# Performance work log

Measured on AMD Instinct MI355X. Metric: run time of the kernel, lower is better.

The kernel has to match this reference:

```python
import jax, jax.numpy as jnp
import numpy as np

B, T, D, H, C = 1024, 128, 13, 512, 9
EPS = 1e-5


def _layer_norm(x, g, b):
    m = x.mean(-1, keepdims=True)
    v = ((x - m) ** 2).mean(-1, keepdims=True)
    return (x - m) / jnp.sqrt(v + EPS) * g + b


def _batch_norm(x, g, b):
    # x: (B, T, H); BatchNorm1d over channel H -> stats over (B, T), biased var
    m = x.mean((0, 1))
    v = ((x - m) ** 2).mean((0, 1))
    return (x - m) / jnp.sqrt(v + EPS) * g + b


def _star_layer(x, WxK, bxK, Wxz, bxz, WhK, bhK, bn_g, bn_b):
    # Precompute input projections for all timesteps (batched GEMMs)
    xK = jnp.einsum('btd,hd->bth', x, WxK) + bxK          # (B,T,H)
    z = jnp.tanh(jnp.einsum('btd,hd->bth', x, Wxz) + bxz)  # (B,T,H)
    h0 = jnp.zeros((x.shape[0], WhK.shape[0]), x.dtype)

    def step(h, inp):
        gK, zt = inp
        K = jax.nn.sigmoid(gK + h @ WhK.T + bhK)
        hn = jnp.tanh(K * h + (1.0 - K) * zt)
        return hn, hn

    _, outs = jax.lax.scan(step, h0, (xK.swapaxes(0, 1), z.swapaxes(0, 1)))
    outs = outs.swapaxes(0, 1)  # (B,T,H)
    return _batch_norm(outs, bn_g, bn_b)


def setup_inputs() -> dict:
    key = jax.random.key(0)
    ks = jax.random.split(key, 10)

    def w(k, o, i):
        return jax.random.normal(k, (o, i), jnp.float32) / np.sqrt(i)

    return {
        'x': jax.random.normal(ks[0], (B, T, D), jnp.float32),
        'inln_g': jnp.ones((D,), jnp.float32),
        'inln_b': jnp.zeros((D,), jnp.float32),
        # layer 1 (input_dim -> H)
        'WxK1': w(ks[1], H, D), 'bxK1': jnp.ones((H,), jnp.float32),
        'Wxz1': w(ks[2], H, D), 'bxz1': jnp.zeros((H,), jnp.float32),
        'WhK1': w(ks[3], H, H), 'bhK1': jnp.zeros((H,), jnp.float32),
        'bn1_g': jnp.ones((H,), jnp.float32), 'bn1_b': jnp.zeros((H,), jnp.float32),
        # layer 2 == layer 3 (shared module instance in the original Sequential)
        'WxK2': w(ks[4], H, H), 'bxK2': jnp.ones((H,), jnp.float32),
        'Wxz2': w(ks[5], H, H), 'bxz2': jnp.zeros((H,), jnp.float32),
        'WhK2': w(ks[6], H, H), 'bhK2': jnp.zeros((H,), jnp.float32),
        'bn2_g': jnp.ones((H,), jnp.float32), 'bn2_b': jnp.zeros((H,), jnp.float32),
        'cln_g': jnp.ones((H,), jnp.float32), 'cln_b': jnp.zeros((H,), jnp.float32),
        'Wc': w(ks[7], C, H), 'bc': jnp.zeros((C,), jnp.float32),
    }


def reference(x, inln_g, inln_b,
              WxK1, bxK1, Wxz1, bxz1, WhK1, bhK1, bn1_g, bn1_b,
              WxK2, bxK2, Wxz2, bxz2, WhK2, bhK2, bn2_g, bn2_b,
              cln_g, cln_b, Wc, bc):
    x = _layer_norm(x, inln_g, inln_b)
    o = _star_layer(x, WxK1, bxK1, Wxz1, bxz1, WhK1, bhK1, bn1_g, bn1_b)
    # layers 2 and 3 share the same weights and batchnorm (duplicated module)
    o = _star_layer(o, WxK2, bxK2, Wxz2, bxz2, WhK2, bhK2, bn2_g, bn2_b)
    o = _star_layer(o, WxK2, bxK2, Wxz2, bxz2, WhK2, bhK2, bn2_g, bn2_b)
    h = _layer_norm(o[:, -1, :], cln_g, cln_b)
    logits = h @ Wc.T + bc
    return jax.nn.log_softmax(logits, axis=-1)
```

## Files before the change

kernel.cpp:

```cpp
#include <hip/hip_runtime.h>
#include <hip/hip_bf16.h>
#include <math.h>

#define B_ 1024
#define T_ 128
#define D_ 13
#define H_ 512
#define C_ 9
#define TC_ 32
#define NC_ (T_/TC_)
#define NT_ (B_*T_)
#define EPS 1e-5f
#define WPAD 520

using frag_ab = __attribute__((ext_vector_type(8))) short;
using frag_cd = __attribute__((ext_vector_type(4))) float;
typedef unsigned short ushort8 __attribute__((ext_vector_type(8)));

static __device__ __forceinline__ float bf2f(unsigned short u){
  union { unsigned int i; float f; } v; v.i = ((unsigned int)u)<<16; return v.f;
}
static __device__ __forceinline__ unsigned short f2bf(float f){
  union { float f; unsigned int i; } v; v.f = f;
  unsigned int r = v.i + 0x7FFF + ((v.i >> 16) & 1);
  return (unsigned short)(r >> 16);
}
static __device__ __forceinline__ float sigmoidf_(float x){ return 1.0f/(1.0f+__expf(-x)); }
static __device__ __forceinline__ float tanhf_(float x){
  return 1.0f - 2.0f/(__expf(2.0f*x)+1.0f);
}

__global__ void k_zero(unsigned int* __restrict__ p, int n){
  int i=blockIdx.x*256+threadIdx.x; if(i<n) p[i]=0u;
}

__global__ void k_swz(const float* __restrict__ Wf, unsigned short* __restrict__ Wz){
  int dst = blockIdx.x*256 + threadIdx.x;
  int w = dst >> 15;
  int i = (dst >> 9) & 63;
  int L = (dst >> 3) & 63;
  int e = dst & 7;
  int kc = i >> 2, c = i & 3;
  int row = w*64 + c*16 + (L & 15);
  int col = kc*32 + ((L >> 4) << 3) + e;
  Wz[dst] = f2bf(Wf[row*H_ + col]);
}

__global__ __launch_bounds__(256) void k_proj1(
    const float* __restrict__ x, const float* __restrict__ g, const float* __restrict__ bvec,
    const float* __restrict__ WxK, const float* __restrict__ bxK,
    const float* __restrict__ Wxz, const float* __restrict__ bxz,
    unsigned short* __restrict__ xKo, unsigned short* __restrict__ zo, int t0)
{
  __shared__ float wK[H_*D_];
  __shared__ float wz[H_*D_];
  __shared__ float xn[TC_][D_];
  int tid = threadIdx.x;
  int b = blockIdx.x;
  const float* xin = x + ((size_t)b*T_ + t0)*D_;
  for(int i=tid;i<H_*D_;i+=256){ wK[i]=WxK[i]; wz[i]=Wxz[i]; }
  for(int i=tid;i<TC_*D_;i+=256){ ((float*)xn)[i] = xin[i]; }
  __syncthreads();
  if(tid<TC_){
    float m=0.f; for(int d=0;d<D_;++d) m+=xn[tid][d]; m*=(1.0f/D_);
    float v=0.f; for(int d=0;d<D_;++d){float t=xn[tid][d]-m; v+=t*t;} v*=(1.0f/D_);
    float inv = rsqrtf(v+EPS);
    for(int d=0;d<D_;++d) xn[tid][d] = (xn[tid][d]-m)*inv*g[d]+bvec[d];
  }
  __syncthreads();
  size_t ob = (size_t)b*TC_*H_;
  for(int hh=0; hh<2; ++hh){
    int h = tid + hh*256;
    float bK = bxK[h], bz = bxz[h];
    for(int r=0;r<TC_;++r){
      float aK=bK, az=bz;
      #pragma unroll
      for(int d=0;d<D_;++d){ float xv = xn[r][d]; aK += xv*wK[h*D_+d]; az += xv*wz[h*D_+d]; }
      xKo[ob + (size_t)r*H_ + h] = f2bf(aK);
      zo [ob + (size_t)r*H_ + h] = f2bf(tanhf_(az));
    }
  }
}

__global__ __launch_bounds__(1024,1) void k_recur8(
    const unsigned short* __restrict__ xK, const unsigned short* __restrict__ z,
    const unsigned short* __restrict__ Wz,
    const float* __restrict__ bhK,
    unsigned short* __restrict__ o,
    float* __restrict__ hbuf,
    float* __restrict__ stats, int t0)
{
  __shared__ __align__(16) unsigned short Wl[8*15*512];
  __shared__ __align__(16) unsigned short hbd[2][16*WPAD];
  int tid=threadIdx.x, lane=tid&63, w=tid>>6;
  int ow=w>>1, oh=w&1;
  int q=lane>>4, cl=lane&15;
  int b0 = blockIdx.x*16;
  const unsigned short* wb = Wz + ((size_t)ow<<15);
  const unsigned short* wl = Wl + ow*7680;
  for(int j=tid;j<7680;j+=1024){
    int wv = j/960, off8 = j%960;
    *(ushort8*)&Wl[wv*7680 + off8*8] = *(const ushort8*)&Wz[((size_t)wv<<15) + off8*8];
  }
  float hp[8];
  float bh[2]; int col[2];
  float ss[2]={0.f,0.f}, qq[2]={0.f,0.f};
  #pragma unroll
  for(int c=0;c<2;++c){ col[c]=ow*64 + (oh*2+c)*16 + cl; bh[c]=bhK[col[c]]; }
  if(t0==0){
    for(int i=tid;i<16*WPAD;i+=1024) hbd[0][i]=0;
    #pragma unroll
    for(int i=0;i<8;++i) hp[i]=0.f;
  } else {
    for(int i=tid;i<16*H_;i+=1024){ int r=i>>9,c=i&511; hbd[0][r*WPAD+c]=f2bf(hbuf[(size_t)(b0+r)*H_+c]); }
    #pragma unroll
    for(int c=0;c<2;++c)
      #pragma unroll
      for(int rg=0;rg<4;++rg) hp[c*4+rg]=hbuf[(size_t)(b0+q*4+rg)*H_+col[c]];
  }
  __syncthreads();
  for(int dt=0;dt<TC_;++dt){
    int cb = dt&1, nb = cb^1;
    float ga[8], za[8];
    #pragma unroll
    for(int c=0;c<2;++c)
      #pragma unroll
      for(int rg=0;rg<4;++rg){
        size_t gi = ((size_t)(b0+q*4+rg)*TC_ + dt)*H_ + col[c];
        ga[c*4+rg]=bf2f(xK[gi]); za[c*4+rg]=bf2f(z[gi]);
      }
    frag_cd acc[2] = {};
    #pragma unroll
    for(int kc=0;kc<16;++kc){
      frag_ab af = *(const frag_ab*)&hbd[cb][cl*WPAD + kc*32 + q*8];
      #pragma unroll
      for(int c=0;c<2;++c){
        int f = kc*4 + oh*2 + c;
        frag_ab bf = (f<15) ? *(const frag_ab*)&wl[f*512 + lane*8]
                            : *(const frag_ab*)&wb[f*512 + lane*8];
        acc[c] = __builtin_amdgcn_mfma_f32_16x16x32_bf16(af, bf, acc[c], 0,0,0);
      }
    }
    unsigned short hnb[8];
    #pragma unroll
    for(int c=0;c<2;++c){
      #pragma unroll
      for(int rg=0;rg<4;++rg){
        int idx = c*4+rg;
        float gv = acc[c][rg] + bh[c] + ga[idx];
        float K  = sigmoidf_(gv);
        float hn = tanhf_(K*hp[idx] + (1.f-K)*za[idx]);
        hp[idx]=hn;
        hnb[idx]=f2bf(hn);
        hbd[nb][(q*4+rg)*WPAD + col[c]] = hnb[idx];
        float hf = bf2f(hnb[idx]);
        ss[c] += hf; qq[c] += hf*hf;
      }
    }
    __syncthreads();
    #pragma unroll
    for(int c=0;c<2;++c)
      #pragma unroll
      for(int rg=0;rg<4;++rg)
        o[((size_t)(b0+q*4+rg)*T_ + t0+dt)*H_ + col[c]] = hnb[c*4+rg];
  }
  #pragma unroll
  for(int c=0;c<2;++c)
    #pragma unroll
    for(int rg=0;rg<4;++rg) hbuf[(size_t)(b0+q*4+rg)*H_+col[c]] = hp[c*4+rg];
  #pragma unroll
  for(int c=0;c<2;++c){
    float s=ss[c], sq=qq[c];
    s  += __shfl_xor(s,16,64);  s  += __shfl_xor(s,32,64);
    sq += __shfl_xor(sq,16,64); sq += __shfl_xor(sq,32,64);
    if(q==0){ atomicAdd(&stats[col[c]], s); atomicAdd(&stats[H_+col[c]], sq); }
  }
}

__global__ void k_foldw(const float* __restrict__ WxK, const float* __restrict__ Wxz,
                        const float* __restrict__ stats, const float* __restrict__ bng,
                        unsigned short* __restrict__ Wp){
  int i = blockIdx.x*256+threadIdx.x;
  int n = i>>9, k = i&511;
  float mean = stats[k]*(1.f/NT_);
  float var  = stats[H_+k]*(1.f/NT_) - mean*mean;
  float s = bng[k]*rsqrtf(var+EPS);
  float wv = (n<H_) ? WxK[(size_t)n*H_+k] : Wxz[(size_t)(n-H_)*H_+k];
  Wp[i] = f2bf(wv*s);
}

__global__ __launch_bounds__(256) void k_foldb(const float* __restrict__ WxK, const float* __restrict__ Wxz,
                        const float* __restrict__ stats, const float* __restrict__ bng, const float* __restrict__ bnb,
                        const float* __restrict__ bxK, const float* __restrict__ bxz,
                        float* __restrict__ biasp){
  int w = threadIdx.x>>6, lane=threadIdx.x&63;
  int n = blockIdx.x*4 + w;
  const float* W = (n<H_) ? &WxK[(size_t)n*H_] : &Wxz[(size_t)(n-H_)*H_];
  float base = (n<H_) ? bxK[n] : bxz[n-H_];
  float acc=0.f;
  for(int k=lane;k<H_;k+=64){
    float mean = stats[k]*(1.f/NT_);
    float var  = stats[H_+k]*(1.f/NT_)-mean*mean;
    float s = bng[k]*rsqrtf(var+EPS);
    float t = bnb[k]-mean*s;
    acc += t*W[k];
  }
  for(int off=32;off;off>>=1) acc += __shfl_down(acc, off, 64);
  if(lane==0) biasp[n] = base + acc;
}

__global__ __launch_bounds__(256) void k_proj23(
    const unsigned short* __restrict__ A,
    const unsigned short* __restrict__ Wp,
    const float* __restrict__ biasp,
    unsigned short* __restrict__ xKo, unsigned short* __restrict__ zo, int t0)
{
  __shared__ __align__(16) unsigned short As[128*32];
  __shared__ __align__(16) unsigned short Bs[128*32];
  int tid=threadIdx.x, lane=tid&63, w=tid>>6;
  int q=lane>>4, cl=lane&15;
  int b0p = blockIdx.x*4;
  int n0 = blockIdx.y*128;
  int wm = (w>>1)*64, wn=(w&1)*64;
  frag_cd acc[4][4] = {};
  int sr = tid>>1, cb = (tid&1)*16;
  size_t arow = ((size_t)(b0p + (sr>>5))*T_ + t0 + (sr&31))*H_;
  size_t brow = (size_t)(n0+sr)*H_;
  for(int k0=0;k0<H_;k0+=32){
    *(frag_ab*)&As[sr*32+cb]   = *(const frag_ab*)&A [arow + k0+cb];
    *(frag_ab*)&As[sr*32+cb+8] = *(const frag_ab*)&A [arow + k0+cb+8];
    *(frag_ab*)&Bs[sr*32+cb]   = *(const frag_ab*)&Wp[brow + k0+cb];
    *(frag_ab*)&Bs[sr*32+cb+8] = *(const frag_ab*)&Wp[brow + k0+cb+8];
    __syncthreads();
    frag_ab af[4], bfr[4];
    #pragma unroll
    for(int mt=0;mt<4;++mt) af[mt]  = *(const frag_ab*)&As[(wm+mt*16+cl)*32 + q*8];
    #pragma unroll
    for(int nt=0;nt<4;++nt) bfr[nt] = *(const frag_ab*)&Bs[(wn+nt*16+cl)*32 + q*8];
    #pragma unroll
    for(int mt=0;mt<4;++mt)
      #pragma unroll
      for(int nt=0;nt<4;++nt)
        acc[mt][nt] = __builtin_amdgcn_mfma_f32_16x16x32_bf16(af[mt], bfr[nt], acc[mt][nt],0,0,0);
    __syncthreads();
  }
  #pragma unroll
  for(int nt=0;nt<4;++nt){
    int coln = n0+wn+nt*16+cl;
    float bp = biasp[coln];
    bool isz = coln>=H_;
    #pragma unroll
    for(int mt=0;mt<4;++mt){
      #pragma unroll
      for(int rg=0;rg<4;++rg){
        int rm = wm+mt*16+q*4+rg;
        size_t orow = (size_t)(b0p*TC_ + rm)*H_;
        float v = acc[mt][nt][rg] + bp;
        if(isz) zo [orow + coln-H_] = f2bf(tanhf_(v));
        else    xKo[orow + coln]    = f2bf(v);
      }
    }
  }
}

__global__ __launch_bounds__(512) void k_head(const unsigned short* __restrict__ o,
     const float* __restrict__ stats, const float* __restrict__ bng, const float* __restrict__ bnb,
     const float* __restrict__ clng, const float* __restrict__ clnb,
     const float* __restrict__ Wc, const float* __restrict__ bc, float* __restrict__ out)
{
  __shared__ float red[8];
  __shared__ float lred[8][9];
  int tid=threadIdx.x, lane=tid&63, w=tid>>6;
  int b = blockIdx.x;
  int c = tid;
  float v = bf2f(o[((size_t)b*T_ + (T_-1))*H_ + c]);
  float mean = stats[c]*(1.f/NT_), var = stats[H_+c]*(1.f/NT_)-mean*mean;
  float s = bng[c]*rsqrtf(var+EPS);
  float y = v*s + (bnb[c]-mean*s);
  float sm=y;
  for(int off=32;off;off>>=1) sm+=__shfl_down(sm,off,64);
  if(lane==0) red[w]=sm;
  __syncthreads();
  float mu=0.f; for(int i=0;i<8;++i) mu+=red[i]; mu*=(1.f/H_);
  float d = y-mu;
  float vq = d*d;
  for(int off=32;off;off>>=1) vq+=__shfl_down(vq,off,64);
  __syncthreads();
  if(lane==0) red[w]=vq;
  __syncthreads();
  float vv=0.f; for(int i=0;i<8;++i) vv+=red[i]; vv*=(1.f/H_);
  float yn = d*rsqrtf(vv+EPS)*clng[c]+clnb[c];
  for(int cls=0;cls<C_;++cls){
    float t = yn*Wc[(size_t)cls*H_+c];
    for(int off=32;off;off>>=1) t+=__shfl_down(t,off,64);
    if(lane==0) lred[w][cls]=t;
  }
  __syncthreads();
  if(tid==0){
    float lg[C_]; float mx=-1e30f;
    for(int cls=0;cls<C_;++cls){
      float t=bc[cls]; for(int i=0;i<8;++i) t+=lred[i][cls];
      lg[cls]=t; mx=fmaxf(mx,t);
    }
    float se=0.f; for(int cls=0;cls<C_;++cls) se+=__expf(lg[cls]-mx);
    float lse=mx+logf(se);
    for(int cls=0;cls<C_;++cls) out[(size_t)b*C_+cls]=lg[cls]-lse;
  }
}

extern "C" void kernel_launch(void* const* d_in, const int* in_sizes, int n_in,
                              void* d_out, int out_size, void* d_ws, size_t ws_size,
                              hipStream_t stream)
{
  (void)in_sizes; (void)n_in; (void)out_size; (void)ws_size;
  const float* x    =(const float*)d_in[0];
  const float* inlng=(const float*)d_in[1];
  const float* inlnb=(const float*)d_in[2];
  const float* WxK1 =(const float*)d_in[3];
  const float* bxK1 =(const float*)d_in[4];
  const float* Wxz1 =(const float*)d_in[5];
  const float* bxz1 =(const float*)d_in[6];
  const float* WhK1 =(const float*)d_in[7];
  const float* bhK1 =(const float*)d_in[8];
  const float* bn1g =(const float*)d_in[9];
  const float* bn1b =(const float*)d_in[10];
  const float* WxK2 =(const float*)d_in[11];
  const float* bxK2 =(const float*)d_in[12];
  const float* Wxz2 =(const float*)d_in[13];
  const float* bxz2 =(const float*)d_in[14];
  const float* WhK2 =(const float*)d_in[15];
  const float* bhK2 =(const float*)d_in[16];
  const float* bn2g =(const float*)d_in[17];
  const float* bn2b =(const float*)d_in[18];
  const float* clng =(const float*)d_in[19];
  const float* clnb =(const float*)d_in[20];
  const float* Wc   =(const float*)d_in[21];
  const float* bc   =(const float*)d_in[22];
  float* out=(float*)d_out;

  char* p=(char*)d_ws;
  unsigned short* o   =(unsigned short*)p; p+=(size_t)NT_*H_*2;
  unsigned short* xK  =(unsigned short*)p; p+=(size_t)B_*TC_*H_*2;
  unsigned short* z   =(unsigned short*)p; p+=(size_t)B_*TC_*H_*2;
  float* hbuf         =(float*)p;          p+=(size_t)B_*H_*4;
  unsigned short* Wz1 =(unsigned short*)p; p+=(size_t)H_*H_*2;
  unsigned short* Wz2 =(unsigned short*)p; p+=(size_t)H_*H_*2;
  unsigned short* Wp  =(unsigned short*)p; p+=(size_t)1024*H_*2;
  float* biasp        =(float*)p;          p+=1024*4;
  float* stats        =(float*)p;          p+=3*1024*4;

  k_zero<<<12,256,0,stream>>>((unsigned int*)stats, 3*1024);
  k_swz<<<H_*H_/256,256,0,stream>>>(WhK1, Wz1);
  k_swz<<<H_*H_/256,256,0,stream>>>(WhK2, Wz2);

  for(int c=0;c<NC_;++c){
    k_proj1<<<B_,256,0,stream>>>(x,inlng,inlnb,WxK1,bxK1,Wxz1,bxz1,xK,z,c*TC_);
    k_recur8<<<64,1024,0,stream>>>(xK,z,Wz1,bhK1,o,hbuf,stats,c*TC_);
  }

  k_foldw<<<1024*H_/256,256,0,stream>>>(WxK2,Wxz2,stats,bn1g,Wp);
  k_foldb<<<256,256,0,stream>>>(WxK2,Wxz2,stats,bn1g,bn1b,bxK2,bxz2,biasp);
  dim3 g23(B_/4, 8);
  for(int c=0;c<NC_;++c){
    k_proj23<<<g23,256,0,stream>>>(o,Wp,biasp,xK,z,c*TC_);
    k_recur8<<<64,1024,0,stream>>>(xK,z,Wz2,bhK2,o,hbuf,stats+1024,c*TC_);
  }

  k_foldw<<<1024*H_/256,256,0,stream>>>(WxK2,Wxz2,stats+1024,bn2g,Wp);
  k_foldb<<<256,256,0,stream>>>(WxK2,Wxz2,stats+1024,bn2g,bn2b,bxK2,bxz2,biasp);
  for(int c=0;c<NC_;++c){
    k_proj23<<<g23,256,0,stream>>>(o,Wp,biasp,xK,z,c*TC_);
    k_recur8<<<64,1024,0,stream>>>(xK,z,Wz2,bhK2,o,hbuf,stats+2048,c*TC_);
  }

  k_head<<<B_,512,0,stream>>>(o, stats+2048, bn2g,bn2b, clng,clnb, Wc,bc, out);
}
```

Before: 3.780 ms.

## Overlap next-chunk projection with recurrence in one fused kernel

Adds a fused kernel where the first 64 blocks run the recurrence for chunk k while up to 192 extra blocks compute the input projections for chunk k+1 into double-buffered xK/z buffers. The aim is to use idle CUs during the latency-bound recurrence and to cut the serialized proj/recur launches. It needs extra workspace and falls back to the old path when the workspace is too small. The projection blocks compete for bandwidth and may slow the recurrence blocks.

```diff
diff --git a/kernel.cpp b/kernel.cpp
--- a/kernel.cpp
+++ b/kernel.cpp
@@ -84,10 +84,8 @@
 
 __global__ __launch_bounds__(1024,1) void k_recur8(
     const unsigned short* __restrict__ xK, const unsigned short* __restrict__ z,
-    const unsigned short* __restrict__ Wz,
-    const float* __restrict__ bhK,
-    unsigned short* __restrict__ o,
-    float* __restrict__ hbuf,
+    const unsigned short* __restrict__ Wz, const float* __restrict__ bhK,
+    unsigned short* __restrict__ o, float* __restrict__ hbuf,
     float* __restrict__ stats, int t0)
 {
   __shared__ __align__(16) unsigned short Wl[8*15*512];
@@ -102,8 +100,7 @@
     int wv = j/960, off8 = j%960;
     *(ushort8*)&Wl[wv*7680 + off8*8] = *(const ushort8*)&Wz[((size_t)wv<<15) + off8*8];
   }
-  float hp[8];
-  float bh[2]; int col[2];
+  float hp[8]; float bh[2]; int col[2];
   float ss[2]={0.f,0.f}, qq[2]={0.f,0.f};
   #pragma unroll
   for(int c=0;c<2;++c){ col[c]=ow*64 + (oh*2+c)*16 + cl; bh[c]=bhK[col[c]]; }
@@ -174,6 +171,202 @@
     s  += __shfl_xor(s,16,64);  s  += __shfl_xor(s,32,64);
     sq += __shfl_xor(sq,16,64); sq += __shfl_xor(sq,32,64);
     if(q==0){ atomicAdd(&stats[col[c]], s); atomicAdd(&stats[H_+col[c]], sq); }
+  }
+}
+
+__global__ __launch_bounds__(1024,1) void k_fused(
+    const unsigned short* __restrict__ xKr, const unsigned short* __restrict__ zr,
+    const unsigned short* __restrict__ Wz, const float* __restrict__ bhK,
+    unsigned short* __restrict__ o, float* __restrict__ hbuf,
+    float* __restrict__ stats, int t0r,
+    int projKind,
+    const unsigned short* __restrict__ Wp, const float* __restrict__ biasp,
+    const float* __restrict__ x, const float* __restrict__ lng, const float* __restrict__ lnb,
+    const float* __restrict__ WxK, const float* __restrict__ bxK,
+    const float* __restrict__ Wxz, const float* __restrict__ bxz,
+    unsigned short* __restrict__ xKo, unsigned short* __restrict__ zo, int t0p)
+{
+  __shared__ __align__(16) unsigned char LDSB[156160];
+  int tid=threadIdx.x;
+  if(blockIdx.x < 64){
+    unsigned short* Wl  = (unsigned short*)LDSB;
+    unsigned short* hbd = (unsigned short*)(LDSB + 122880);
+    int lane=tid&63, w=tid>>6;
+    int ow=w>>1, oh=w&1;
+    int q=lane>>4, cl=lane&15;
+    int b0 = blockIdx.x*16;
+    const unsigned short* wb = Wz + ((size_t)ow<<15);
+    const unsigned short* wl = Wl + ow*7680;
+    for(int j=tid;j<7680;j+=1024){
+      int wv = j/960, off8 = j%960;
+      *(ushort8*)&Wl[wv*7680 + off8*8] = *(const ushort8*)&Wz[((size_t)wv<<15) + off8*8];
+    }
+    float hp[8]; float bh[2]; int col[2];
+    float ss[2]={0.f,0.f}, qq[2]={0.f,0.f};
+    #pragma unroll
+    for(int c=0;c<2;++c){ col[c]=ow*64 + (oh*2+c)*16 + cl; bh[c]=bhK[col[c]]; }
+    if(t0r==0){
+      for(int i=tid;i<16*WPAD;i+=1024) hbd[i]=0;
+      #pragma unroll
+      for(int i=0;i<8;++i) hp[i]=0.f;
+    } else {
+      for(int i=tid;i<16*H_;i+=1024){ int r=i>>9,c=i&511; hbd[r*WPAD+c]=f2bf(hbuf[(size_t)(b0+r)*H_+c]); }
+      #pragma unroll
+      for(int c=0;c<2;++c)
+        #pragma unroll
+        for(int rg=0;rg<4;++rg) hp[c*4+rg]=hbuf[(size_t)(b0+q*4+rg)*H_+col[c]];
+    }
+    __syncthreads();
+    for(int dt=0;dt<TC_;++dt){
+      int cb = dt&1, nb = cb^1;
+      float ga[8], za[8];
+      #pragma unroll
+      for(int c=0;c<2;++c)
+        #pragma unroll
+        for(int rg=0;rg<4;++rg){
+          size_t gi = ((size_t)(b0+q*4+rg)*TC_ + dt)*H_ + col[c];
+          ga[c*4+rg]=bf2f(xKr[gi]); za[c*4+rg]=bf2f(zr[gi]);
+        }
+      frag_cd acc[2] = {};
+      #pragma unroll
+      for(int kc=0;kc<16;++kc){
+        frag_ab af = *(const frag_ab*)&hbd[cb*16*WPAD + cl*WPAD + kc*32 + q*8];
+        #pragma unroll
+        for(int c=0;c<2;++c){
+          int f = kc*4 + oh*2 + c;
+          frag_ab bf = (f<15) ? *(const frag_ab*)&wl[f*512 + lane*8]
+                              : *(const frag_ab*)&wb[f*512 + lane*8];
+          acc[c] = __builtin_amdgcn_mfma_f32_16x16x32_bf16(af, bf, acc[c], 0,0,0);
+        }
+      }
+      unsigned short hnb[8];
+      #pragma unroll
+      for(int c=0;c<2;++c){
+        #pragma unroll
+        for(int rg=0;rg<4;++rg){
+          int idx = c*4+rg;
+          float gv = acc[c][rg] + bh[c] + ga[idx];
+          float K  = sigmoidf_(gv);
+          float hn = tanhf_(K*hp[idx] + (1.f-K)*za[idx]);
+          hp[idx]=hn;
+          hnb[idx]=f2bf(hn);
+          hbd[nb*16*WPAD + (q*4+rg)*WPAD + col[c]] = hnb[idx];
+          float hf = bf2f(hnb[idx]);
+          ss[c] += hf; qq[c] += hf*hf;
+        }
+      }
+      __syncthreads();
+      #pragma unroll
+      for(int c=0;c<2;++c)
+        #pragma unroll
+        for(int rg=0;rg<4;++rg)
+          o[((size_t)(b0+q*4+rg)*T_ + t0r+dt)*H_ + col[c]] = hnb[c*4+rg];
+    }
+    #pragma unroll
+    for(int c=0;c<2;++c)
+      #pragma unroll
+      for(int rg=0;rg<4;++rg) hbuf[(size_t)(b0+q*4+rg)*H_+col[c]] = hp[c*4+rg];
+    #pragma unroll
+    for(int c=0;c<2;++c){
+      float s=ss[c], sq=qq[c];
+      s  += __shfl_xor(s,16,64);  s  += __shfl_xor(s,32,64);
+      sq += __shfl_xor(sq,16,64); sq += __shfl_xor(sq,32,64);
+      if(q==0){ atomicAdd(&stats[col[c]], s); atomicAdd(&stats[H_+col[c]], sq); }
+    }
+  } else if(projKind == 2){
+    int s = tid>>8, stid = tid&255;
+    unsigned short* As = (unsigned short*)(LDSB + s*16384);
+    unsigned short* Bs = (unsigned short*)(LDSB + s*16384 + 8192);
+    int lane=stid&63, w4=stid>>6;
+    int q=lane>>4, cl=lane&15;
+    int eng = (int)(blockIdx.x-64)*4 + s;
+    for(int it=0; it<3; ++it){
+      int tile = eng + it*768;
+      bool valid = tile < 2048;
+      int vt = valid ? tile : 0;
+      int mt = vt>>3, ntl = vt&7;
+      int b0p = mt*4, n0 = ntl*128;
+      int wm = (w4>>1)*64, wn=(w4&1)*64;
+      frag_cd acc[4][4] = {};
+      int sr = stid>>1, cb2 = (stid&1)*16;
+      size_t arow = ((size_t)(b0p + (sr>>5))*T_ + t0p + (sr&31))*H_;
+      size_t brow = (size_t)(n0+sr)*H_;
+      for(int k0=0;k0<H_;k0+=32){
+        *(frag_ab*)&As[sr*32+cb2]   = *(const frag_ab*)&o [arow + k0+cb2];
+        *(frag_ab*)&As[sr*32+cb2+8] = *(const frag_ab*)&o [arow + k0+cb2+8];
+        *(frag_ab*)&Bs[sr*32+cb2]   = *(const frag_ab*)&Wp[brow + k0+cb2];
+        *(frag_ab*)&Bs[sr*32+cb2+8] = *(const frag_ab*)&Wp[brow + k0+cb2+8];
+        __syncthreads();
+        frag_ab af[4], bfr[4];
+        #pragma unroll
+        for(int mi=0;mi<4;++mi) af[mi]  = *(const frag_ab*)&As[(wm+mi*16+cl)*32 + q*8];
+        #pragma unroll
+        for(int ni=0;ni<4;++ni) bfr[ni] = *(const frag_ab*)&Bs[(wn+ni*16+cl)*32 + q*8];
+        #pragma unroll
+        for(int mi=0;mi<4;++mi)
+          #pragma unroll
+          for(int ni=0;ni<4;++ni)
+            acc[mi][ni] = __builtin_amdgcn_mfma_f32_16x16x32_bf16(af[mi], bfr[ni], acc[mi][ni],0,0,0);
+        __syncthreads();
+      }
+      if(valid){
+        #pragma unroll
+        for(int ni=0;ni<4;++ni){
+          int coln = n0+wn+ni*16+cl;
+          float bp = biasp[coln];
+          bool isz = coln>=H_;
+          #pragma unroll
+          for(int mi=0;mi<4;++mi){
+            #pragma unroll
+            for(int rg=0;rg<4;++rg){
+              int rm = wm+mi*16+q*4+rg;
+              size_t orow = (size_t)(b0p*TC_ + rm)*H_;
+              float v = acc[mi][ni][rg] + bp;
+              if(isz) zo [orow + coln-H_] = f2bf(tanhf_(v));
+              else    xKo[orow + coln]    = f2bf(v);
+            }
+          }
+        }
+      }
+    }
+  } else if(projKind == 1){
+    float* wKs = (float*)LDSB;
+    float* wzs = (float*)(LDSB + 26624);
+    int s = tid>>8, stid = tid&255;
+    float* xns = (float*)(LDSB + 53248 + s*1664);
+    for(int i=tid;i<H_*D_;i+=1024){ wKs[i]=WxK[i]; wzs[i]=Wxz[i]; }
+    __syncthreads();
+    int eng = (int)(blockIdx.x-64)*4 + s;
+    for(int it=0; it<2; ++it){
+      int row = eng + it*768;
+      bool valid = row < B_;
+      int b = valid ? row : 0;
+      const float* xin = x + ((size_t)b*T_ + t0p)*D_;
+      for(int i=stid;i<TC_*D_;i+=256) xns[i] = xin[i];
+      __syncthreads();
+      if(stid<TC_){
+        float m=0.f; for(int d=0;d<D_;++d) m+=xns[stid*D_+d]; m*=(1.0f/D_);
+        float v=0.f; for(int d=0;d<D_;++d){float t=xns[stid*D_+d]-m; v+=t*t;} v*=(1.0f/D_);
+        float inv = rsqrtf(v+EPS);
+        for(int d=0;d<D_;++d) xns[stid*D_+d] = (xns[stid*D_+d]-m)*inv*lng[d]+lnb[d];
+      }
+      __syncthreads();
+      size_t ob = (size_t)b*TC_*H_;
+      for(int hh=0; hh<2; ++hh){
+        int h = stid + hh*256;
+        float bK = bxK[h], bz = bxz[h];
+        for(int r=0;r<TC_;++r){
+          float aK=bK, az=bz;
+          #pragma unroll
+          for(int d=0;d<D_;++d){ float xv = xns[r*D_+d]; aK += xv*wKs[h*D_+d]; az += xv*wzs[h*D_+d]; }
+          if(valid){
+            xKo[ob + (size_t)r*H_ + h] = f2bf(aK);
+            zo [ob + (size_t)r*H_ + h] = f2bf(tanhf_(az));
+          }
+        }
+      }
+      __syncthreads();
+    }
   }
 }
 
@@ -312,7 +505,7 @@
                               void* d_out, int out_size, void* d_ws, size_t ws_size,
                               hipStream_t stream)
 {
-  (void)in_sizes; (void)n_in; (void)out_size; (void)ws_size;
+  (void)in_sizes; (void)n_in; (void)out_size;
   const float* x    =(const float*)d_in[0];
   const float* inlng=(const float*)d_in[1];
   const float* inlnb=(const float*)d_in[2];
@@ -338,10 +531,18 @@
   const float* bc   =(const float*)d_in[22];
   float* out=(float*)d_out;
 
+  const size_t NEED_FUSED = 272646144ull;
+  bool fused = ws_size >= NEED_FUSED;
+
   char* p=(char*)d_ws;
-  unsigned short* o   =(unsigned short*)p; p+=(size_t)NT_*H_*2;
-  unsigned short* xK  =(unsigned short*)p; p+=(size_t)B_*TC_*H_*2;
-  unsigned short* z   =(unsigned short*)p; p+=(size_t)B_*TC_*H_*2;
+  unsigned short* o = (unsigned short*)p; p+=(size_t)NT_*H_*2;
+  unsigned short* xKb[2]; unsigned short* zb[2];
+  xKb[0]=(unsigned short*)p; p+=(size_t)B_*TC_*H_*2;
+  zb[0] =(unsigned short*)p; p+=(size_t)B_*TC_*H_*2;
+  if(fused){
+    xKb[1]=(unsigned short*)p; p+=(size_t)B_*TC_*H_*2;
+    zb[1] =(unsigned short*)p; p+=(size_t)B_*TC_*H_*2;
+  } else { xKb[1]=xKb[0]; zb[1]=zb[0]; }
   float* hbuf         =(float*)p;          p+=(size_t)B_*H_*4;
   unsigned short* Wz1 =(unsigned short*)p; p+=(size_t)H_*H_*2;
   unsigned short* Wz2 =(unsigned short*)p; p+=(size_t)H_*H_*2;
@@ -353,24 +554,53 @@
   k_swz<<<H_*H_/256,256,0,stream>>>(WhK1, Wz1);
   k_swz<<<H_*H_/256,256,0,stream>>>(WhK2, Wz2);
 
-  for(int c=0;c<NC_;++c){
-    k_proj1<<<B_,256,0,stream>>>(x,inlng,inlnb,WxK1,bxK1,Wxz1,bxz1,xK,z,c*TC_);
-    k_recur8<<<64,1024,0,stream>>>(xK,z,Wz1,bhK1,o,hbuf,stats,c*TC_);
-  }
-
-  k_foldw<<<1024*H_/256,256,0,stream>>>(WxK2,Wxz2,stats,bn1g,Wp);
-  k_foldb<<<256,256,0,stream>>>(WxK2,Wxz2,stats,bn1g,bn1b,bxK2,bxz2,biasp);
   dim3 g23(B_/4, 8);
-  for(int c=0;c<NC_;++c){
-    k_proj23<<<g23,256,0,stream>>>(o,Wp,biasp,xK,z,c*TC_);
-    k_recur8<<<64,1024,0,stream>>>(xK,z,Wz2,bhK2,o,hbuf,stats+1024,c*TC_);
-  }
-
-  k_foldw<<<1024*H_/256,256,0,stream>>>(WxK2,Wxz2,stats+1024,bn2g,Wp);
-  k_foldb<<<256,256,0,stream>>>(WxK2,Wxz2,stats+1024,bn2g,bn2b,bxK2,bxz2,biasp);
-  for(int c=0;c<NC_;++c){
-    k_proj23<<<g23,256,0,stream>>>(o,Wp,biasp,xK,z,c*TC_);
-    k_recur8<<<64,1024,0,stream>>>(xK,z,Wz2,bhK2,o,hbuf,stats+2048,c*TC_);
+  if(fused){
+    k_proj1<<<B_,256,0,stream>>>(x,inlng,inlnb,WxK1,bxK1,Wxz1,bxz1,xKb[0],zb[0],0);
+    for(int k=0;k<NC_;++k){
+      int kind = (k<NC_-1) ? 1 : 0;
+      int grid = 64 + (kind?192:0);
+      k_fused<<<grid,1024,0,stream>>>(xKb[k&1],zb[k&1],Wz1,bhK1,o,hbuf,stats,k*TC_,
+          kind, Wp,biasp, x,inlng,inlnb, WxK1,bxK1,Wxz1,bxz1,
+          xKb[(k+1)&1],zb[(k+1)&1],(k+1)*TC_);
+    }
+    k_foldw<<<1024*H_/256,256,0,stream>>>(WxK2,Wxz2,stats,bn1g,Wp);
+    k_foldb<<<256,256,0,stream>>>(WxK2,Wxz2,stats,bn1g,bn1b,bxK2,bxz2,biasp);
+    k_proj23<<<g23,256,0,stream>>>(o,Wp,biasp,xKb[0],zb[0],0);
+    for(int k=0;k<NC_;++k){
+      int kind = (k<NC_-1) ? 2 : 0;
+      int grid = 64 + (kind?192:0);
+      k_fused<<<grid,1024,0,stream>>>(xKb[k&1],zb[k&1],Wz2,bhK2,o,hbuf,stats+1024,k*TC_,
+          kind, Wp,biasp, x,inlng,inlnb, WxK1,bxK1,Wxz1,bxz1,
+          xKb[(k+1)&1],zb[(k+1)&1],(k+1)*TC_);
+    }
+    k_foldw<<<1024*H_/256,256,0,stream>>>(WxK2,Wxz2,stats+1024,bn2g,Wp);
+    k_foldb<<<256,256,0,stream>>>(WxK2,Wxz2,stats+1024,bn2g,bn2b,bxK2,bxz2,biasp);
+    k_proj23<<<g23,256,0,stream>>>(o,Wp,biasp,xKb[0],zb[0],0);
+    for(int k=0;k<NC_;++k){
+      int kind = (k<NC_-1) ? 2 : 0;
+      int grid = 64 + (kind?192:0);
+      k_fused<<<grid,1024,0,stream>>>(xKb[k&1],zb[k&1],Wz2,bhK2,o,hbuf,stats+2048,k*TC_,
+          kind, Wp,biasp, x,inlng,inlnb, WxK1,bxK1,Wxz1,bxz1,
+          xKb[(k+1)&1],zb[(k+1)&1],(k+1)*TC_);
+    }
+  } else {
+    for(int c=0;c<NC_;++c){
+      k_proj1<<<B_,256,0,stream>>>(x,inlng,inlnb,WxK1,bxK1,Wxz1,bxz1,xKb[0],zb[0],c*TC_);
+      k_recur8<<<64,1024,0,stream>>>(xKb[0],zb[0],Wz1,bhK1,o,hbuf,stats,c*TC_);
+    }
+    k_foldw<<<1024*H_/256,256,0,stream>>>(WxK2,Wxz2,stats,bn1g,Wp);
+    k_foldb<<<256,256,0,stream>>>(WxK2,Wxz2,stats,bn1g,bn1b,bxK2,bxz2,biasp);
+    for(int c=0;c<NC_;++c){
+      k_proj23<<<g23,256,0,stream>>>(o,Wp,biasp,xKb[0],zb[0],c*TC_);
+      k_recur8<<<64,1024,0,stream>>>(xKb[0],zb[0],Wz2,bhK2,o,hbuf,stats+1024,c*TC_);
+    }
+    k_foldw<<<1024*H_/256,256,0,stream>>>(WxK2,Wxz2,stats+1024,bn2g,Wp);
+    k_foldb<<<256,256,0,stream>>>(WxK2,Wxz2,stats+1024,bn2g,bn2b,bxK2,bxz2,biasp);
+    for(int c=0;c<NC_;++c){
+      k_proj23<<<g23,256,0,stream>>>(o,Wp,biasp,xKb[0],zb[0],c*TC_);
+      k_recur8<<<64,1024,0,stream>>>(xKb[0],zb[0],Wz2,bhK2,o,hbuf,stats+2048,c*TC_);
+    }
   }
 
   k_head<<<B_,512,0,stream>>>(o, stats+2048, bn2g,bn2b, clng,clnb, Wc,bc, out);
```

Result: no change. 3.772 ms (-0.2%).

## Overlap next-chunk input projection with recurrence in one fused kernel using flags

Applied to the files above, without the earlier changes.

Merges the per-chunk recurrence and the next chunk's input projection into a single launch. The first 64 blocks run the recurrence, and 192 extra blocks compute the next chunk's xK/z projection (LayerNorm+small GEMM for layer 1, MFMA GEMM for layers 2/3). The recurrence blocks bump global flags every 4 timesteps, and the projection blocks spin on those flags before overwriting the shared xK/z buffers. The aim is to hide projection time behind the serial recurrence and use CUs the recurrence leaves idle. The cost is spin-wait synchronization that depends on all blocks being co-resident, plus extra code complexity.

```diff
diff --git a/kernel.cpp b/kernel.cpp
--- a/kernel.cpp
+++ b/kernel.cpp
@@ -28,6 +28,17 @@
 static __device__ __forceinline__ float sigmoidf_(float x){ return 1.0f/(1.0f+__expf(-x)); }
 static __device__ __forceinline__ float tanhf_(float x){
   return 1.0f - 2.0f/(__expf(2.0f*x)+1.0f);
+}
+static __device__ __forceinline__ void waitflag(const unsigned int* f, unsigned int tgt){
+  int lane = threadIdx.x & 63;
+  unsigned int v;
+  do {
+    v = 0u;
+    if(lane==0) v = __hip_atomic_load(f, __ATOMIC_RELAXED, __HIP_MEMORY_SCOPE_AGENT);
+    v = __shfl((int)v, 0, 64);
+    if(v < tgt) __builtin_amdgcn_s_sleep(8);
+  } while(v < tgt);
+  asm volatile("" ::: "memory");
 }
 
 __global__ void k_zero(unsigned int* __restrict__ p, int n){
@@ -82,98 +93,205 @@
   }
 }
 
-__global__ __launch_bounds__(1024,1) void k_recur8(
-    const unsigned short* __restrict__ xK, const unsigned short* __restrict__ z,
-    const unsigned short* __restrict__ Wz,
-    const float* __restrict__ bhK,
-    unsigned short* __restrict__ o,
-    float* __restrict__ hbuf,
-    float* __restrict__ stats, int t0)
+__global__ __launch_bounds__(1024,1) void k_fused(
+    const unsigned short* xKr, const unsigned short* zr,
+    const unsigned short* __restrict__ Wz, const float* __restrict__ bhK,
+    unsigned short* __restrict__ o, float* __restrict__ hbuf,
+    float* __restrict__ stats, int t0r,
+    int projKind,
+    const unsigned short* __restrict__ Wp, const float* __restrict__ biasp,
+    const float* __restrict__ x, const float* __restrict__ lng, const float* __restrict__ lnb,
+    const float* __restrict__ WxK, const float* __restrict__ bxK,
+    const float* __restrict__ Wxz, const float* __restrict__ bxz,
+    unsigned short* xKo, unsigned short* zo, int t0p,
+    unsigned int* flagp)
 {
-  __shared__ __align__(16) unsigned short Wl[8*15*512];
-  __shared__ __align__(16) unsigned short hbd[2][16*WPAD];
-  int tid=threadIdx.x, lane=tid&63, w=tid>>6;
-  int ow=w>>1, oh=w&1;
-  int q=lane>>4, cl=lane&15;
-  int b0 = blockIdx.x*16;
-  const unsigned short* wb = Wz + ((size_t)ow<<15);
-  const unsigned short* wl = Wl + ow*7680;
-  for(int j=tid;j<7680;j+=1024){
-    int wv = j/960, off8 = j%960;
-    *(ushort8*)&Wl[wv*7680 + off8*8] = *(const ushort8*)&Wz[((size_t)wv<<15) + off8*8];
-  }
-  float hp[8];
-  float bh[2]; int col[2];
-  float ss[2]={0.f,0.f}, qq[2]={0.f,0.f};
-  #pragma unroll
-  for(int c=0;c<2;++c){ col[c]=ow*64 + (oh*2+c)*16 + cl; bh[c]=bhK[col[c]]; }
-  if(t0==0){
-    for(int i=tid;i<16*WPAD;i+=1024) hbd[0][i]=0;
-    #pragma unroll
-    for(int i=0;i<8;++i) hp[i]=0.f;
-  } else {
-    for(int i=tid;i<16*H_;i+=1024){ int r=i>>9,c=i&511; hbd[0][r*WPAD+c]=f2bf(hbuf[(size_t)(b0+r)*H_+c]); }
+  __shared__ __align__(16) unsigned char LDSB[156160];
+  int tid=threadIdx.x;
+  if(blockIdx.x < 64){
+    unsigned short* Wl  = (unsigned short*)LDSB;
+    unsigned short* hbd = (unsigned short*)(LDSB + 122880);
+    int lane=tid&63, w=tid>>6;
+    int ow=w>>1, oh=w&1;
+    int q=lane>>4, cl=lane&15;
+    int b0 = blockIdx.x*16;
+    const unsigned short* wb = Wz + ((size_t)ow<<15);
+    const unsigned short* wl = Wl + ow*7680;
+    for(int j=tid;j<7680;j+=1024){
+      int wv = j/960, off8 = j%960;
+      *(ushort8*)&Wl[wv*7680 + off8*8] = *(const ushort8*)&Wz[((size_t)wv<<15) + off8*8];
+    }
+    float hp[8]; float bh[2]; int col[2];
+    float ss[2]={0.f,0.f}, qq[2]={0.f,0.f};
+    #pragma unroll
+    for(int c=0;c<2;++c){ col[c]=ow*64 + (oh*2+c)*16 + cl; bh[c]=bhK[col[c]]; }
+    if(t0r==0){
+      for(int i=tid;i<16*WPAD;i+=1024) hbd[i]=0;
+      #pragma unroll
+      for(int i=0;i<8;++i) hp[i]=0.f;
+    } else {
+      for(int i=tid;i<16*H_;i+=1024){ int r=i>>9,c=i&511; hbd[r*WPAD+c]=f2bf(hbuf[(size_t)(b0+r)*H_+c]); }
+      #pragma unroll
+      for(int c=0;c<2;++c)
+        #pragma unroll
+        for(int rg=0;rg<4;++rg) hp[c*4+rg]=hbuf[(size_t)(b0+q*4+rg)*H_+col[c]];
+    }
+    __syncthreads();
+    for(int dt=0;dt<TC_;++dt){
+      int cb = dt&1, nb = cb^1;
+      float ga[8], za[8];
+      #pragma unroll
+      for(int c=0;c<2;++c)
+        #pragma unroll
+        for(int rg=0;rg<4;++rg){
+          size_t gi = ((size_t)(b0+q*4+rg)*TC_ + dt)*H_ + col[c];
+          ga[c*4+rg]=bf2f(xKr[gi]); za[c*4+rg]=bf2f(zr[gi]);
+        }
+      frag_cd acc[2] = {};
+      #pragma unroll
+      for(int kc=0;kc<16;++kc){
+        frag_ab af = *(const frag_ab*)&hbd[cb*16*WPAD + cl*WPAD + kc*32 + q*8];
+        #pragma unroll
+        for(int c=0;c<2;++c){
+          int f = kc*4 + oh*2 + c;
+          frag_ab bf = (f<15) ? *(const frag_ab*)&wl[f*512 + lane*8]
+                              : *(const frag_ab*)&wb[f*512 + lane*8];
+          acc[c] = __builtin_amdgcn_mfma_f32_16x16x32_bf16(af, bf, acc[c], 0,0,0);
+        }
+      }
+      unsigned short hnb[8];
+      #pragma unroll
+      for(int c=0;c<2;++c){
+        #pragma unroll
+        for(int rg=0;rg<4;++rg){
+          int idx = c*4+rg;
+          float gv = acc[c][rg] + bh[c] + ga[idx];
+          float K  = sigmoidf_(gv);
+          float hn = tanhf_(K*hp[idx] + (1.f-K)*za[idx]);
+          hp[idx]=hn;
+          hnb[idx]=f2bf(hn);
+          hbd[nb*16*WPAD + (q*4+rg)*WPAD + col[c]] = hnb[idx];
+          float hf = bf2f(hnb[idx]);
+          ss[c] += hf; qq[c] += hf*hf;
+        }
+      }
+      __syncthreads();
+      if(((dt&3)==3) && tid==0) atomicAdd(&flagp[dt>>2], 1u);
+      #pragma unroll
+      for(int c=0;c<2;++c)
+        #pragma unroll
+        for(int rg=0;rg<4;++rg)
+          o[((size_t)(b0+q*4+rg)*T_ + t0r+dt)*H_ + col[c]] = hnb[c*4+rg];
+    }
     #pragma unroll
     for(int c=0;c<2;++c)
       #pragma unroll
-      for(int rg=0;rg<4;++rg) hp[c*4+rg]=hbuf[(size_t)(b0+q*4+rg)*H_+col[c]];
-  }
-  __syncthreads();
-  for(int dt=0;dt<TC_;++dt){
-    int cb = dt&1, nb = cb^1;
-    float ga[8], za[8];
-    #pragma unroll
-    for(int c=0;c<2;++c)
-      #pragma unroll
-      for(int rg=0;rg<4;++rg){
-        size_t gi = ((size_t)(b0+q*4+rg)*TC_ + dt)*H_ + col[c];
-        ga[c*4+rg]=bf2f(xK[gi]); za[c*4+rg]=bf2f(z[gi]);
-      }
-    frag_cd acc[2] = {};
-    #pragma unroll
-    for(int kc=0;kc<16;++kc){
-      frag_ab af = *(const frag_ab*)&hbd[cb][cl*WPAD + kc*32 + q*8];
-      #pragma unroll
-      for(int c=0;c<2;++c){
-        int f = kc*4 + oh*2 + c;
-        frag_ab bf = (f<15) ? *(const frag_ab*)&wl[f*512 + lane*8]
-                            : *(const frag_ab*)&wb[f*512 + lane*8];
-        acc[c] = __builtin_amdgcn_mfma_f32_16x16x32_bf16(af, bf, acc[c], 0,0,0);
-      }
-    }
-    unsigned short hnb[8];
+      for(int rg=0;rg<4;++rg) hbuf[(size_t)(b0+q*4+rg)*H_+col[c]] = hp[c*4+rg];
     #pragma unroll
     for(int c=0;c<2;++c){
-      #pragma unroll
-      for(int rg=0;rg<4;++rg){
-        int idx = c*4+rg;
-        float gv = acc[c][rg] + bh[c] + ga[idx];
-        float K  = sigmoidf_(gv);
-        float hn = tanhf_(K*hp[idx] + (1.f-K)*za[idx]);
-        hp[idx]=hn;
-        hnb[idx]=f2bf(hn);
-        hbd[nb][(q*4+rg)*WPAD + col[c]] = hnb[idx];
-        float hf = bf2f(hnb[idx]);
-        ss[c] += hf; qq[c] += hf*hf;
-      }
-    }
+      float s=ss[c], sq=qq[c];
+      s  += __shfl_xor(s,16,64);  s  += __shfl_xor(s,32,64);
+      sq += __shfl_xor(sq,16,64); sq += __shfl_xor(sq,32,64);
+      if(q==0){ atomicAdd(&stats[col[c]], s); atomicAdd(&stats[H_+col[c]], sq); }
+    }
+  } else if(projKind == 2){
+    int s = tid>>8, stid = tid&255;
+    unsigned short* As = (unsigned short*)(LDSB + s*16384);
+    unsigned short* Bs = (unsigned short*)(LDSB + s*16384 + 8192);
+    int lane=stid&63, w4=stid>>6;
+    int q=lane>>4, cl=lane&15;
+    int eng = (int)(blockIdx.x-64)*4 + s;
+    for(int it=0; it<3; ++it){
+      int t = eng + it*768;
+      bool valid = t < 2048;
+      int vt = valid ? t : 0;
+      int g = vt>>8, idx = vt&255;
+      int b32 = (idx>>3)*32, n0 = (idx&7)*128;
+      int wm = (w4>>1)*64, wn=(w4&1)*64;
+      frag_cd acc[4][4] = {};
+      int sr = stid>>1, cb2 = (stid&1)*16;
+      size_t arow = ((size_t)(b32 + (sr>>2))*T_ + t0p + g*4 + (sr&3))*H_;
+      size_t brow = (size_t)(n0+sr)*H_;
+      for(int k0=0;k0<H_;k0+=32){
+        *(frag_ab*)&As[sr*32+cb2]   = *(const frag_ab*)&o [arow + k0+cb2];
+        *(frag_ab*)&As[sr*32+cb2+8] = *(const frag_ab*)&o [arow + k0+cb2+8];
+        *(frag_ab*)&Bs[sr*32+cb2]   = *(const frag_ab*)&Wp[brow + k0+cb2];
+        *(frag_ab*)&Bs[sr*32+cb2+8] = *(const frag_ab*)&Wp[brow + k0+cb2+8];
+        __syncthreads();
+        frag_ab af[4], bfr[4];
+        #pragma unroll
+        for(int mi=0;mi<4;++mi) af[mi]  = *(const frag_ab*)&As[(wm+mi*16+cl)*32 + q*8];
+        #pragma unroll
+        for(int ni=0;ni<4;++ni) bfr[ni] = *(const frag_ab*)&Bs[(wn+ni*16+cl)*32 + q*8];
+        #pragma unroll
+        for(int mi=0;mi<4;++mi)
+          #pragma unroll
+          for(int ni=0;ni<4;++ni)
+            acc[mi][ni] = __builtin_amdgcn_mfma_f32_16x16x32_bf16(af[mi], bfr[ni], acc[mi][ni],0,0,0);
+        __syncthreads();
+      }
+      if(valid){
+        waitflag(&flagp[g], 64u);
+        #pragma unroll
+        for(int ni=0;ni<4;++ni){
+          int coln = n0+wn+ni*16+cl;
+          float bp = biasp[coln];
+          bool isz = coln>=H_;
+          #pragma unroll
+          for(int mi=0;mi<4;++mi){
+            #pragma unroll
+            for(int rg=0;rg<4;++rg){
+              int rm = wm+mi*16+q*4+rg;
+              size_t orow = ((size_t)(b32 + (rm>>2))*TC_ + g*4 + (rm&3))*H_;
+              float v = acc[mi][ni][rg] + bp;
+              if(isz) zo [orow + coln-H_] = f2bf(tanhf_(v));
+              else    xKo[orow + coln]    = f2bf(v);
+            }
+          }
+        }
+      }
+    }
+  } else if(projKind == 1){
+    float* wKs = (float*)LDSB;
+    float* wzs = (float*)(LDSB + 26624);
+    int s = tid>>8, stid = tid&255;
+    float* xns = (float*)(LDSB + 53248 + s*1664);
+    for(int i=tid;i<H_*D_;i+=1024){ wKs[i]=WxK[i]; wzs[i]=Wxz[i]; }
     __syncthreads();
-    #pragma unroll
-    for(int c=0;c<2;++c)
-      #pragma unroll
-      for(int rg=0;rg<4;++rg)
-        o[((size_t)(b0+q*4+rg)*T_ + t0+dt)*H_ + col[c]] = hnb[c*4+rg];
-  }
-  #pragma unroll
-  for(int c=0;c<2;++c)
-    #pragma unroll
-    for(int rg=0;rg<4;++rg) hbuf[(size_t)(b0+q*4+rg)*H_+col[c]] = hp[c*4+rg];
-  #pragma unroll
-  for(int c=0;c<2;++c){
-    float s=ss[c], sq=qq[c];
-    s  += __shfl_xor(s,16,64);  s  += __shfl_xor(s,32,64);
-    sq += __shfl_xor(sq,16,64); sq += __shfl_xor(sq,32,64);
-    if(q==0){ atomicAdd(&stats[col[c]], s); atomicAdd(&stats[H_+col[c]], sq); }
+    int eng = (int)(blockIdx.x-64)*4 + s;
+    for(int it=0; it<2; ++it){
+      int row = eng + it*768;
+      bool valid = row < B_;
+      int b = valid ? row : 0;
+      const float* xin = x + ((size_t)b*T_ + t0p)*D_;
+      for(int i=stid;i<TC_*D_;i+=256) xns[i] = xin[i];
+      __syncthreads();
+      if(stid<TC_){
+        float m=0.f; for(int d=0;d<D_;++d) m+=xns[stid*D_+d]; m*=(1.0f/D_);
+        float v=0.f; for(int d=0;d<D_;++d){float t2=xns[stid*D_+d]-m; v+=t2*t2;} v*=(1.0f/D_);
+        float inv = rsqrtf(v+EPS);
+        for(int d=0;d<D_;++d) xns[stid*D_+d] = (xns[stid*D_+d]-m)*inv*lng[d]+lnb[d];
+      }
+      __syncthreads();
+      size_t ob = (size_t)b*TC_*H_;
+      for(int g=0; g<8; ++g){
+        if(valid) waitflag(&flagp[g], 64u);
+        for(int hh=0; hh<2; ++hh){
+          int h = stid + hh*256;
+          float bK = bxK[h], bz = bxz[h];
+          for(int r=g*4; r<g*4+4; ++r){
+            float aK=bK, az=bz;
+            #pragma unroll
+            for(int d=0;d<D_;++d){ float xv = xns[r*D_+d]; aK += xv*wKs[h*D_+d]; az += xv*wzs[h*D_+d]; }
+            if(valid){
+              xKo[ob + (size_t)r*H_ + h] = f2bf(aK);
+              zo [ob + (size_t)r*H_ + h] = f2bf(tanhf_(az));
+            }
+          }
+        }
+      }
+      __syncthreads();
+    }
   }
 }
 
@@ -348,30 +466,35 @@
   unsigned short* Wp  =(unsigned short*)p; p+=(size_t)1024*H_*2;
   float* biasp        =(float*)p;          p+=1024*4;
   float* stats        =(float*)p;          p+=3*1024*4;
-
-  k_zero<<<12,256,0,stream>>>((unsigned int*)stats, 3*1024);
+  unsigned int* flags =(unsigned int*)p;   p+=12*8*4;
+
+  k_zero<<<13,256,0,stream>>>((unsigned int*)stats, 3*1024 + 12*8);
   k_swz<<<H_*H_/256,256,0,stream>>>(WhK1, Wz1);
   k_swz<<<H_*H_/256,256,0,stream>>>(WhK2, Wz2);
 
-  for(int c=0;c<NC_;++c){
-    k_proj1<<<B_,256,0,stream>>>(x,inlng,inlnb,WxK1,bxK1,Wxz1,bxz1,xK,z,c*TC_);
-    k_recur8<<<64,1024,0,stream>>>(xK,z,Wz1,bhK1,o,hbuf,stats,c*TC_);
-  }
-
+  dim3 g23(B_/4, 8);
+  int ci = 0;
+  k_proj1<<<B_,256,0,stream>>>(x,inlng,inlnb,WxK1,bxK1,Wxz1,bxz1,xK,z,0);
+  for(int k=0;k<NC_;++k,++ci){
+    int kind = (k<NC_-1) ? 1 : 0;
+    k_fused<<<64+(kind?192:0),1024,0,stream>>>(xK,z,Wz1,bhK1,o,hbuf,stats,k*TC_,
+        kind, Wp,biasp, x,inlng,inlnb, WxK1,bxK1,Wxz1,bxz1, xK,z,(k+1)*TC_, flags+ci*8);
+  }
   k_foldw<<<1024*H_/256,256,0,stream>>>(WxK2,Wxz2,stats,bn1g,Wp);
   k_foldb<<<256,256,0,stream>>>(WxK2,Wxz2,stats,bn1g,bn1b,bxK2,bxz2,biasp);
-  dim3 g23(B_/4, 8);
-  for(int c=0;c<NC_;++c){
-    k_proj23<<<g23,256,0,stream>>>(o,Wp,biasp,xK,z,c*TC_);
-    k_recur8<<<64,1024,0,stream>>>(xK,z,Wz2,bhK2,o,hbuf,stats+1024,c*TC_);
-  }
-
+  k_proj23<<<g23,256,0,stream>>>(o,Wp,biasp,xK,z,0);
+  for(int k=0;k<NC_;++k,++ci){
+    int kind = (k<NC_-1) ? 2 : 0;
+    k_fused<<<64+(kind?192:0),1024,0,stream>>>(xK,z,Wz2,bhK2,o,hbuf,stats+1024,k*TC_,
+        kind, Wp,biasp, x,inlng,inlnb, WxK1,bxK1,Wxz1,bxz1, xK,z,(k+1)*TC_, flags+ci*8);
+  }
   k_foldw<<<1024*H_/256,256,0,stream>>>(WxK2,Wxz2,stats+1024,bn2g,Wp);
   k_foldb<<<256,256,0,stream>>>(WxK2,Wxz2,stats+1024,bn2g,bn2b,bxK2,bxz2,biasp);
-  for(int c=0;c<NC_;++c){
-    k_proj23<<<g23,256,0,stream>>>(o,Wp,biasp,xK,z,c*TC_);
-    k_recur8<<<64,1024,0,stream>>>(xK,z,Wz2,bhK2,o,hbuf,stats+2048,c*TC_);
-  }
-
+  k_proj23<<<g23,256,0,stream>>>(o,Wp,biasp,xK,z,0);
+  for(int k=0;k<NC_;++k,++ci){
+    int kind = (k<NC_-1) ? 2 : 0;
+    k_fused<<<64+(kind?192:0),1024,0,stream>>>(xK,z,Wz2,bhK2,o,hbuf,stats+2048,k*TC_,
+        kind, Wp,biasp, x,inlng,inlnb, WxK1,bxK1,Wxz1,bxz1, xK,z,(k+1)*TC_, flags+ci*8);
+  }
   k_head<<<B_,512,0,stream>>>(o, stats+2048, bn2g,bn2b, clng,clnb, Wc,bc, out);
 }
```

Result: slower. 4.534 ms (+20.0%).
